# Performance work log

Hardware: AMD Instinct MI355X
Metric: run time of the kernel (lower is better)

## Reference

```python
import jax, jax.numpy as jnp
import numpy as np
from math import factorial

# (mul, l, parity) in mul_ir layout order
IRREPS_IN1 = [(128, 0, 1), (128, 1, -1), (128, 2, 1)]
IRREPS_IN2 = [(1, 0, 1), (1, 1, -1), (1, 2, 1)]
IRREPS_OUT = [(128, 0, 1), (128, 1, -1), (128, 2, 1)]
BATCH = 65536


def _f(n):
    return float(factorial(int(round(n))))


def _su2_cg(j1, j2, j3, m1, m2, m3):
    # <j1 m1 j2 m2 | j3 m3> (Racah formula, complex SU(2) basis)
    if m3 != m1 + m2:
        return 0.0
    vmin = int(max(-j1 + j2 + m3, -j1 + m1, 0))
    vmax = int(min(j2 + j3 + m1, j3 - j1 + j2, j3 + m3))
    C = ((2 * j3 + 1) * _f(j3 + j1 - j2) * _f(j3 - j1 + j2) * _f(j1 + j2 - j3)
         * _f(j3 + m3) * _f(j3 - m3)
         / (_f(j1 + j2 + j3 + 1) * _f(j1 - m1) * _f(j1 + m1) * _f(j2 - m2) * _f(j2 + m2))) ** 0.5
    S = 0.0
    for v in range(vmin, vmax + 1):
        S += (-1.0) ** (v + j2 + m2) * _f(j2 + j3 + m1 - v) * _f(j1 - m1 + v) / (
            _f(v) * _f(j3 - j1 + j2 - v) * _f(j3 + m3 - v) * _f(v + j1 - j2 - m3))
    return C * S


def _q(l):
    # change of basis real -> complex spherical harmonics (e3nn convention)
    q = np.zeros((2 * l + 1, 2 * l + 1), dtype=np.complex128)
    for m in range(-l, 0):
        q[l + m, l + abs(m)] = 1 / np.sqrt(2)
        q[l + m, l - abs(m)] = -1j / np.sqrt(2)
    q[l, l] = 1.0
    for m in range(1, l + 1):
        q[l + m, l + abs(m)] = (-1) ** m / np.sqrt(2)
        q[l + m, l - abs(m)] = 1j * (-1) ** m / np.sqrt(2)
    return (-1j) ** l * q


def _wigner_3j(l1, l2, l3):
    C = np.zeros((2 * l1 + 1, 2 * l2 + 1, 2 * l3 + 1))
    for m1 in range(-l1, l1 + 1):
        for m2 in range(-l2, l2 + 1):
            for m3 in range(-l3, l3 + 1):
                C[l1 + m1, l2 + m2, l3 + m3] = _su2_cg(l1, l2, l3, m1, m2, m3)
    Q1, Q2, Q3 = _q(l1), _q(l2), _q(l3)
    R = np.einsum('ij,kl,nm,ikn->jlm', Q1, Q2, np.conj(Q3), C.astype(np.complex128))
    return np.real(R) / np.sqrt(2 * l3 + 1)  # sum of squares == 1 (3j normalization)


def _slices(irreps):
    out, off = [], 0
    for mul, l, _ in irreps:
        out.append((off, mul, 2 * l + 1))
        off += mul * (2 * l + 1)
    return out, off


S1, DIM1 = _slices(IRREPS_IN1)
S2, DIM2 = _slices(IRREPS_IN2)
S3, DIM3 = _slices(IRREPS_OUT)

# fully-connected instruction list: all parity/triangle-allowed (i1, i2, i3) paths
_instr = [(i1, i2, i3)
          for i1, (_, l1, p1) in enumerate(IRREPS_IN1)
          for i2, (_, l2, p2) in enumerate(IRREPS_IN2)
          for i3, (_, l3, p3) in enumerate(IRREPS_OUT)
          if p1 * p2 == p3 and abs(l1 - l2) <= l3 <= l1 + l2]

# path normalization 'element': fan-in per output irrep = sum of mul1*mul2 over incoming paths
_fan = {}
for i1, i2, i3 in _instr:
    _fan[i3] = _fan.get(i3, 0) + IRREPS_IN1[i1][0] * IRREPS_IN2[i2][0]

PATHS, _off = [], 0
for i1, i2, i3 in _instr:
    mu1, l1, _ = IRREPS_IN1[i1]
    mu2, l2, _ = IRREPS_IN2[i2]
    mu3, l3, _ = IRREPS_OUT[i3]
    # irrep_normalization 'component' + path 'element': path_weight = sqrt((2l3+1)/fan)
    cg = _wigner_3j(l1, l2, l3) * np.sqrt((2 * l3 + 1) / _fan[i3])
    PATHS.append((i1, i2, i3, _off, (mu1, mu2, mu3), jnp.asarray(cg, dtype=jnp.float32)))
    _off += mu1 * mu2 * mu3
WEIGHT_NUMEL = _off  # 180224 for these irreps (11 paths x 128*1*128)


def _fctp(x1, x2, weight):
    w = weight.reshape(-1).astype(x1.dtype)
    acc = [None] * len(IRREPS_OUT)
    for i1, i2, i3, off, wshape, cg in PATHS:
        o1, mu1, d1 = S1[i1]
        o2, mu2, d2 = S2[i2]
        a = x1[:, o1:o1 + mu1 * d1].reshape(-1, mu1, d1)  # [B, u, i]
        b = x2[:, o2:o2 + mu2 * d2].reshape(-1, mu2, d2)  # [B, v, j]
        wp = w[off:off + wshape[0] * wshape[1] * wshape[2]].reshape(wshape)  # [u, v, w]
        c = jnp.einsum('bui,bvj,uvw,ijk->bwk', a, b, wp, cg.astype(x1.dtype))
        acc[i3] = c if acc[i3] is None else acc[i3] + c
    # mul_ir layout: flatten each (B, mul, 2l+1) segment and concatenate
    return jnp.concatenate([s.reshape(s.shape[0], -1) for s in acc], axis=-1)


def setup_inputs():
    key = jax.random.key(0)
    k1, k2, k3 = jax.random.split(key, 3)
    return {
        "x1": jax.random.normal(k1, (BATCH, DIM1), dtype=jnp.float32),
        "x2": jax.random.normal(k2, (BATCH, DIM2), dtype=jnp.float32),
        "weight": jax.random.normal(k3, (1, WEIGHT_NUMEL), dtype=jnp.float32),
    }


def reference(x1, x2, weight):
    return _fctp(x1, x2, weight)
```

## Files before the change

kernel.cpp:

```cpp
#include <hip/hip_runtime.h>
#include <hip/hip_bf16.h>

typedef __attribute__((ext_vector_type(8))) short bf16x8;
typedef __attribute__((ext_vector_type(4))) float f32x4;
typedef __attribute__((ext_vector_type(4))) unsigned int u32x4;
typedef __attribute__((ext_vector_type(2))) unsigned int u32x2;
typedef __attribute__((ext_vector_type(4))) unsigned short u16x4;

__device__ __forceinline__ unsigned short f2bf(float f) {
  __hip_bfloat16 h = __float2bfloat16(f);
  return __builtin_bit_cast(unsigned short, h);
}
__device__ __forceinline__ float bfw(unsigned int word, int hi) {
  union { unsigned int i; float f; } v;
  v.i = hi ? (word & 0xffff0000u) : (word << 16);
  return v.f;
}

struct cplx { double re, im; };
__device__ __forceinline__ cplx cmul(cplx a, cplx b) {
  return {a.re * b.re - a.im * b.im, a.re * b.im + a.im * b.re};
}
__device__ __forceinline__ double fct_(int n) {
  const double f[8] = {1., 1., 2., 6., 24., 120., 720., 5040.};
  return f[n];
}
__device__ __forceinline__ int imax_(int a, int b) { return a > b ? a : b; }
__device__ __forceinline__ int imin_(int a, int b) { return a < b ? a : b; }

__device__ double su2_cg(int j1, int j2, int j3, int m1, int m2, int m3) {
  if (m3 != m1 + m2) return 0.0;
  int vmin = imax_(imax_(-j1 + j2 + m3, -j1 + m1), 0);
  int vmax = imin_(imin_(j2 + j3 + m1, j3 - j1 + j2), j3 + m3);
  double C = sqrt((2.0 * j3 + 1.0) * fct_(j3 + j1 - j2) * fct_(j3 - j1 + j2) * fct_(j1 + j2 - j3)
                  * fct_(j3 + m3) * fct_(j3 - m3)
                  / (fct_(j1 + j2 + j3 + 1) * fct_(j1 - m1) * fct_(j1 + m1) * fct_(j2 - m2) * fct_(j2 + m2)));
  double S = 0.0;
  for (int v = vmin; v <= vmax; ++v) {
    double sgn = ((v + j2 + m2) & 1) ? -1.0 : 1.0;
    S += sgn * fct_(j2 + j3 + m1 - v) * fct_(j1 - m1 + v)
         / (fct_(v) * fct_(j3 - j1 + j2 - v) * fct_(j3 + m3 - v) * fct_(v + j1 - j2 - m3));
  }
  return C * S;
}

__device__ cplx q_entry(int l, int r, int c) {
  const double s2 = 0.70710678118654752440;
  int m = r - l;
  cplx v = {0.0, 0.0};
  if (m < 0) {
    if (c == l - m) v = {s2, 0.0};
    else if (c == l + m) v = {0.0, -s2};
  } else if (m == 0) {
    if (c == l) v = {1.0, 0.0};
  } else {
    double sgn = (m & 1) ? -1.0 : 1.0;
    if (c == l + m) v = {sgn * s2, 0.0};
    else if (c == l - m) v = {0.0, sgn * s2};
  }
  cplx f;
  switch (l & 3) {
    case 0: f = {1.0, 0.0}; break;
    case 1: f = {0.0, -1.0}; break;
    case 2: f = {-1.0, 0.0}; break;
    default: f = {0.0, 1.0}; break;
  }
  return cmul(f, v);
}

__global__ void init_kernel(const float* __restrict__ w, unsigned short* __restrict__ Wt,
                            float* __restrict__ cgw, float* __restrict__ gfold,
                            unsigned int* __restrict__ gmap) {
  const int blk = blockIdx.x;
  const int tid = threadIdx.x;
  if (blk < 704) {
    int g = blk * 256 + tid;
    int p = g >> 14, rem = g & 16383;
    int u = rem >> 7, wc = rem & 127;
    Wt[(p << 14) + (wc << 7) + u] = f2bf(w[g]);
    return;
  }
  if (blk == 715) {
    if (tid < 115) {
      const int PBt[12] = {0,1,4,9,18,21,36,45,70,85,90,115};
      const int O2t[11] = {0,1,4,0,1,1,4,0,1,4,4};
      int p = 0;
      while (tid >= PBt[p + 1]) ++p;
      gmap[tid] = O2t[p];
    }
    return;
  }
  __shared__ float s_cg[125];
  const int p = blk - 704;
  const int L1t[11] = {0,0,0,1,1,1,1,2,2,2,2};
  const int L2t[11] = {0,1,2,0,1,1,2,0,1,2,2};
  const int L3t[11] = {0,1,2,1,0,2,1,2,1,0,2};
  const int PBt[11] = {0,1,4,9,18,21,36,45,70,85,90};
  const double FAN[11] = {384.,512.,512.,512.,384.,512.,512.,512.,512.,384.,512.};
  const int l1 = L1t[p], l2 = L2t[p], l3 = L3t[p];
  const int n1 = 2 * l1 + 1, n2 = 2 * l2 + 1, n3 = 2 * l3 + 1;
  if (tid < n1 * n2 * n3) {
    const int a = tid / (n2 * n3), b = (tid / n3) % n2, c = tid % n3;
    double sre = 0.0;
    for (int i = 0; i < n1; ++i)
      for (int k = 0; k < n2; ++k)
        for (int n = 0; n < n3; ++n) {
          double cg = su2_cg(l1, l2, l3, i - l1, k - l2, n - l3);
          if (cg == 0.0) continue;
          cplx q1 = q_entry(l1, i, a);
          cplx q2 = q_entry(l2, k, b);
          cplx q3 = q_entry(l3, n, c);
          q3.im = -q3.im;
          cplx pr = cmul(cmul(q1, q2), q3);
          sre += pr.re * cg;
        }
    float val = (float)(sre / sqrt(FAN[p]));
    s_cg[a * 25 + b * 5 + c] = val;
    cgw[p * 125 + a * 25 + b * 5 + c] = val;
  }
  __syncthreads();
  if (tid < n1 * n3) {
    int i = tid / n3, k = tid % n3;
    for (int j = 0; j < 5; ++j)
      gfold[(PBt[p] + tid) * 5 + j] = (j < n2) ? s_cg[i * 25 + j * 5 + k] : 0.f;
  }
}

__device__ __forceinline__ void stage_all(const float* __restrict__ x1, int Mbase,
                                          unsigned short* __restrict__ s_a) {
  const int tid = threadIdx.x;
#pragma unroll 4
  for (int rep = 0; rep < 18; ++rep) {
    int it = tid + rep * 256;
    int row = it / 288, c4 = it % 288;
    int col = c4 << 2;
    const f32x4 v = __builtin_nontemporal_load(
        (const f32x4*)&x1[(size_t)(Mbase + row) * 1152 + col]);
    unsigned short* sr = s_a + row * 128;
    if (col < 128) {
      u16x4 h;
#pragma unroll
      for (int q = 0; q < 4; ++q) h[q] = f2bf(v[q]);
      *(u16x4*)&sr[(((col >> 3) ^ row) << 3) + (col & 7)] = h;
    } else if (col < 512) {
      int cc = col - 128;
#pragma unroll
      for (int q = 0; q < 4; ++q) {
        int u = (cc + q) / 3, i = (cc + q) % 3;
        s_a[(1 + i) * 2048 + row * 128 + (((u >> 3) ^ row) << 3) + (u & 7)] = f2bf(v[q]);
      }
    } else {
      int cc = col - 512;
#pragma unroll
      for (int q = 0; q < 4; ++q) {
        int u = (cc + q) / 5, i = (cc + q) % 5;
        s_a[(4 + i) * 2048 + row * 128 + (((u >> 3) ^ row) << 3) + (u & 7)] = f2bf(v[q]);
      }
    }
  }
}

template<int PID, int L1, int L3, int PBASE>
__device__ __forceinline__ void do_path(const unsigned short* __restrict__ s_a,
                                        const unsigned short* __restrict__ s_g,
                                        const unsigned short* __restrict__ Wt,
                                        int kg, int r16, int nbase,
                                        f32x4 (&acc)[2 * L3 + 1][2]) {
  constexpr int D1 = 2 * L1 + 1, D3 = 2 * L3 + 1;
  constexpr int GB = (L1 == 0) ? 0 : ((L1 == 1) ? 2048 : 8192);
  const unsigned short* __restrict__ wbase = Wt + (PID << 14);
  u32x4 bw[2][4];
#pragma unroll
  for (int nf = 0; nf < 2; ++nf)
#pragma unroll
    for (int us = 0; us < 4; ++us)
      bw[nf][us] = *(const u32x4*)&wbase[(nbase + nf * 16 + r16) * 128 + us * 32 + kg * 8];
  const unsigned short* __restrict__ ap0 = s_a + GB + r16 * 128;
  auto gread = [&](int e) -> f32x4 {
    const u32x2 gd = *(const u32x2*)&s_g[(e << 4) + (kg << 2)];
    f32x4 r;
    r[0] = bfw(gd.x, 0); r[1] = bfw(gd.x, 1);
    r[2] = bfw(gd.y, 0); r[3] = bfw(gd.y, 1);
    return r;
  };
#pragma unroll 1
  for (int ii = 0; ii + 1 < D1; ii += 2) {
    const unsigned short* apA = ap0 + ii * 2048;
    const unsigned short* apB = apA + 2048;
    f32x4 y0[2][2] = {{f32x4{0.f,0.f,0.f,0.f}, f32x4{0.f,0.f,0.f,0.f}},
                      {f32x4{0.f,0.f,0.f,0.f}, f32x4{0.f,0.f,0.f,0.f}}};
    f32x4 y1[2][2] = {{f32x4{0.f,0.f,0.f,0.f}, f32x4{0.f,0.f,0.f,0.f}},
                      {f32x4{0.f,0.f,0.f,0.f}, f32x4{0.f,0.f,0.f,0.f}}};
#pragma unroll
    for (int us = 0; us < 4; ++us) {
      const int soff = (((us * 4 + kg) ^ r16) << 3);
      const u32x4 a0 = *(const u32x4*)(apA + soff);
      const u32x4 a1 = *(const u32x4*)(apB + soff);
      const int h = us & 1;
#pragma unroll
      for (int nf = 0; nf < 2; ++nf) {
        y0[nf][h] = __builtin_amdgcn_mfma_f32_16x16x32_bf16(
            __builtin_bit_cast(bf16x8, a0), __builtin_bit_cast(bf16x8, bw[nf][us]),
            y0[nf][h], 0, 0, 0);
        y1[nf][h] = __builtin_amdgcn_mfma_f32_16x16x32_bf16(
            __builtin_bit_cast(bf16x8, a1), __builtin_bit_cast(bf16x8, bw[nf][us]),
            y1[nf][h], 0, 0, 0);
      }
    }
#pragma unroll
    for (int k = 0; k < D3; ++k) {
      const f32x4 gA = gread(PBASE + ii * D3 + k);
      const f32x4 gB = gread(PBASE + (ii + 1) * D3 + k);
#pragma unroll
      for (int nf = 0; nf < 2; ++nf) {
        acc[k][nf] += gA * (y0[nf][0] + y0[nf][1]);
        acc[k][nf] += gB * (y1[nf][0] + y1[nf][1]);
      }
    }
  }
  if (D1 & 1) {
    constexpr int it = D1 - 1;
    const unsigned short* ap = ap0 + it * 2048;
    f32x4 y[2][2] = {{f32x4{0.f,0.f,0.f,0.f}, f32x4{0.f,0.f,0.f,0.f}},
                     {f32x4{0.f,0.f,0.f,0.f}, f32x4{0.f,0.f,0.f,0.f}}};
#pragma unroll
    for (int us = 0; us < 4; ++us) {
      const int soff = (((us * 4 + kg) ^ r16) << 3);
      const u32x4 af = *(const u32x4*)(ap + soff);
      const int h = us & 1;
#pragma unroll
      for (int nf = 0; nf < 2; ++nf)
        y[nf][h] = __builtin_amdgcn_mfma_f32_16x16x32_bf16(
            __builtin_bit_cast(bf16x8, af), __builtin_bit_cast(bf16x8, bw[nf][us]),
            y[nf][h], 0, 0, 0);
    }
#pragma unroll
    for (int k = 0; k < D3; ++k) {
      const f32x4 g4 = gread(PBASE + it * D3 + k);
#pragma unroll
      for (int nf = 0; nf < 2; ++nf) acc[k][nf] += g4 * (y[nf][0] + y[nf][1]);
    }
  }
}

__global__ void __launch_bounds__(256, 2) fctp_main(
    const float* __restrict__ x1, const float* __restrict__ x2,
    const float* __restrict__ gfold, const unsigned int* __restrict__ gmap,
    const unsigned short* __restrict__ Wt, float* __restrict__ out) {
  __shared__ __align__(16) unsigned short s_a[18432];
  __shared__ __align__(16) unsigned short s_g[1840];
  const int tid = threadIdx.x;
  const int Mbase = blockIdx.x << 4;

  stage_all(x1, Mbase, s_a);

  {
    const int row = tid & 15, e0 = tid >> 4;
    const float* __restrict__ xr = x2 + (size_t)(Mbase + row) * 9;
    float x2r[9];
#pragma unroll
    for (int j = 0; j < 9; ++j) x2r[j] = xr[j];
#pragma unroll
    for (int it = 0; it < 8; ++it) {
      const int e = e0 + it * 16;
      if (e < 115) {
        const int o2 = (int)gmap[e];
        const float* __restrict__ gf = gfold + e * 5;
        float s = 0.f;
#pragma unroll
        for (int j = 0; j < 5; ++j) s += gf[j] * x2r[o2 + j];
        s_g[(e << 4) + row] = f2bf(s);
      }
    }
  }

  const int lane = tid & 63, ni = tid >> 6;
  const int r16 = lane & 15, kg = lane >> 4;
  const int nbase = ni << 5;

  __syncthreads();

  const int bout = Mbase + (kg << 2);

  {
    f32x4 acc[1][2] = {};
    do_path<0, 0, 0, 0>(s_a, s_g, Wt, kg, r16, nbase, acc);
    do_path<4, 1, 0, 18>(s_a, s_g, Wt, kg, r16, nbase, acc);
    do_path<9, 2, 0, 85>(s_a, s_g, Wt, kg, r16, nbase, acc);
#pragma unroll
    for (int nf = 0; nf < 2; ++nf) {
      const int w = nbase + nf * 16 + r16;
#pragma unroll
      for (int r = 0; r < 4; ++r)
        __builtin_nontemporal_store(acc[0][nf][r],
                                    &out[(size_t)(bout + r) * 1152 + w]);
    }
  }
  {
    f32x4 acc[3][2] = {};
    do_path<1, 0, 1, 1>(s_a, s_g, Wt, kg, r16, nbase, acc);
    do_path<3, 1, 1, 9>(s_a, s_g, Wt, kg, r16, nbase, acc);
    do_path<6, 1, 1, 36>(s_a, s_g, Wt, kg, r16, nbase, acc);
    do_path<8, 2, 1, 70>(s_a, s_g, Wt, kg, r16, nbase, acc);
#pragma unroll
    for (int nf = 0; nf < 2; ++nf) {
      const int w = nbase + nf * 16 + r16;
#pragma unroll
      for (int r = 0; r < 4; ++r) {
        float* o = out + (size_t)(bout + r) * 1152 + 128 + w * 3;
#pragma unroll
        for (int k = 0; k < 3; ++k) o[k] = acc[k][nf][r];
      }
    }
  }
  {
    f32x4 acc[5][2] = {};
    do_path<2, 0, 2, 4>(s_a, s_g, Wt, kg, r16, nbase, acc);
    do_path<5, 1, 2, 21>(s_a, s_g, Wt, kg, r16, nbase, acc);
    do_path<7, 2, 2, 45>(s_a, s_g, Wt, kg, r16, nbase, acc);
    do_path<10, 2, 2, 90>(s_a, s_g, Wt, kg, r16, nbase, acc);
#pragma unroll
    for (int nf = 0; nf < 2; ++nf) {
      const int w = nbase + nf * 16 + r16;
#pragma unroll
      for (int r = 0; r < 4; ++r) {
        float* o = out + (size_t)(bout + r) * 1152 + 512 + w * 5;
#pragma unroll
        for (int k = 0; k < 5; ++k) o[k] = acc[k][nf][r];
      }
    }
  }
}

extern "C" void kernel_launch(void* const* d_in, const int* in_sizes, int n_in,
                              void* d_out, int out_size, void* d_ws, size_t ws_size,
                              hipStream_t stream) {
  (void)in_sizes; (void)n_in; (void)out_size; (void)ws_size;
  const float* x1 = (const float*)d_in[0];
  const float* x2 = (const float*)d_in[1];
  const float* w  = (const float*)d_in[2];
  float* out = (float*)d_out;
  float* cgw = (float*)d_ws;
  unsigned int* gmap = (unsigned int*)((char*)d_ws + 5504);
  float* gfold = (float*)((char*)d_ws + 6144);
  unsigned short* Wt = (unsigned short*)((char*)d_ws + 16384);
  init_kernel<<<dim3(716), dim3(256), 0, stream>>>(w, Wt, cgw, gfold, gmap);
  fctp_main<<<dim3(4096), dim3(256), 0, stream>>>(x1, x2, gfold, gmap, Wt, out);
}
```

Before: 330.8 us.

## Split output channels across two blocks per row tile, halving per-wave N work

```diff
diff --git a/kernel.cpp b/kernel.cpp
--- a/kernel.cpp
+++ b/kernel.cpp
@@ -134,8 +134,7 @@
     int it = tid + rep * 256;
     int row = it / 288, c4 = it % 288;
     int col = c4 << 2;
-    const f32x4 v = __builtin_nontemporal_load(
-        (const f32x4*)&x1[(size_t)(Mbase + row) * 1152 + col]);
+    const f32x4 v = *(const f32x4*)&x1[(size_t)(Mbase + row) * 1152 + col];
     unsigned short* sr = s_a + row * 128;
     if (col < 128) {
       u16x4 h;
@@ -165,16 +164,14 @@
                                         const unsigned short* __restrict__ s_g,
                                         const unsigned short* __restrict__ Wt,
                                         int kg, int r16, int nbase,
-                                        f32x4 (&acc)[2 * L3 + 1][2]) {
+                                        f32x4 (&acc)[2 * L3 + 1]) {
   constexpr int D1 = 2 * L1 + 1, D3 = 2 * L3 + 1;
   constexpr int GB = (L1 == 0) ? 0 : ((L1 == 1) ? 2048 : 8192);
   const unsigned short* __restrict__ wbase = Wt + (PID << 14);
-  u32x4 bw[2][4];
-#pragma unroll
-  for (int nf = 0; nf < 2; ++nf)
-#pragma unroll
-    for (int us = 0; us < 4; ++us)
-      bw[nf][us] = *(const u32x4*)&wbase[(nbase + nf * 16 + r16) * 128 + us * 32 + kg * 8];
+  u32x4 bw[4];
+#pragma unroll
+  for (int us = 0; us < 4; ++us)
+    bw[us] = *(const u32x4*)&wbase[(nbase + r16) * 128 + us * 32 + kg * 8];
   const unsigned short* __restrict__ ap0 = s_a + GB + r16 * 128;
   auto gread = [&](int e) -> f32x4 {
     const u32x2 gd = *(const u32x2*)&s_g[(e << 4) + (kg << 2)];
@@ -187,58 +184,46 @@
   for (int ii = 0; ii + 1 < D1; ii += 2) {
     const unsigned short* apA = ap0 + ii * 2048;
     const unsigned short* apB = apA + 2048;
-    f32x4 y0[2][2] = {{f32x4{0.f,0.f,0.f,0.f}, f32x4{0.f,0.f,0.f,0.f}},
-                      {f32x4{0.f,0.f,0.f,0.f}, f32x4{0.f,0.f,0.f,0.f}}};
-    f32x4 y1[2][2] = {{f32x4{0.f,0.f,0.f,0.f}, f32x4{0.f,0.f,0.f,0.f}},
-                      {f32x4{0.f,0.f,0.f,0.f}, f32x4{0.f,0.f,0.f,0.f}}};
+    f32x4 y0[2] = {f32x4{0.f,0.f,0.f,0.f}, f32x4{0.f,0.f,0.f,0.f}};
+    f32x4 y1[2] = {f32x4{0.f,0.f,0.f,0.f}, f32x4{0.f,0.f,0.f,0.f}};
 #pragma unroll
     for (int us = 0; us < 4; ++us) {
       const int soff = (((us * 4 + kg) ^ r16) << 3);
       const u32x4 a0 = *(const u32x4*)(apA + soff);
       const u32x4 a1 = *(const u32x4*)(apB + soff);
-      const int h = us & 1;
-#pragma unroll
-      for (int nf = 0; nf < 2; ++nf) {
-        y0[nf][h] = __builtin_amdgcn_mfma_f32_16x16x32_bf16(
-            __builtin_bit_cast(bf16x8, a0), __builtin_bit_cast(bf16x8, bw[nf][us]),
-            y0[nf][h], 0, 0, 0);
-        y1[nf][h] = __builtin_amdgcn_mfma_f32_16x16x32_bf16(
-            __builtin_bit_cast(bf16x8, a1), __builtin_bit_cast(bf16x8, bw[nf][us]),
-            y1[nf][h], 0, 0, 0);
-      }
+      const int hh = us & 1;
+      y0[hh] = __builtin_amdgcn_mfma_f32_16x16x32_bf16(
+          __builtin_bit_cast(bf16x8, a0), __builtin_bit_cast(bf16x8, bw[us]),
+          y0[hh], 0, 0, 0);
+      y1[hh] = __builtin_amdgcn_mfma_f32_16x16x32_bf16(
+          __builtin_bit_cast(bf16x8, a1), __builtin_bit_cast(bf16x8, bw[us]),
+          y1[hh], 0, 0, 0);
     }
 #pragma unroll
     for (int k = 0; k < D3; ++k) {
       const f32x4 gA = gread(PBASE + ii * D3 + k);
       const f32x4 gB = gread(PBASE + (ii + 1) * D3 + k);
-#pragma unroll
-      for (int nf = 0; nf < 2; ++nf) {
-        acc[k][nf] += gA * (y0[nf][0] + y0[nf][1]);
-        acc[k][nf] += gB * (y1[nf][0] + y1[nf][1]);
-      }
+      acc[k] += gA * (y0[0] + y0[1]);
+      acc[k] += gB * (y1[0] + y1[1]);
     }
   }
   if (D1 & 1) {
     constexpr int it = D1 - 1;
     const unsigned short* ap = ap0 + it * 2048;
-    f32x4 y[2][2] = {{f32x4{0.f,0.f,0.f,0.f}, f32x4{0.f,0.f,0.f,0.f}},
-                     {f32x4{0.f,0.f,0.f,0.f}, f32x4{0.f,0.f,0.f,0.f}}};
+    f32x4 y[2] = {f32x4{0.f,0.f,0.f,0.f}, f32x4{0.f,0.f,0.f,0.f}};
 #pragma unroll
     for (int us = 0; us < 4; ++us) {
       const int soff = (((us * 4 + kg) ^ r16) << 3);
       const u32x4 af = *(const u32x4*)(ap + soff);
-      const int h = us & 1;
-#pragma unroll
-      for (int nf = 0; nf < 2; ++nf)
-        y[nf][h] = __builtin_amdgcn_mfma_f32_16x16x32_bf16(
-            __builtin_bit_cast(bf16x8, af), __builtin_bit_cast(bf16x8, bw[nf][us]),
-            y[nf][h], 0, 0, 0);
+      const int hh = us & 1;
+      y[hh] = __builtin_amdgcn_mfma_f32_16x16x32_bf16(
+          __builtin_bit_cast(bf16x8, af), __builtin_bit_cast(bf16x8, bw[us]),
+          y[hh], 0, 0, 0);
     }
 #pragma unroll
     for (int k = 0; k < D3; ++k) {
       const f32x4 g4 = gread(PBASE + it * D3 + k);
-#pragma unroll
-      for (int nf = 0; nf < 2; ++nf) acc[k][nf] += g4 * (y[nf][0] + y[nf][1]);
+      acc[k] += g4 * (y[0] + y[1]);
     }
   }
 }
@@ -250,7 +235,8 @@
   __shared__ __align__(16) unsigned short s_a[18432];
   __shared__ __align__(16) unsigned short s_g[1840];
   const int tid = threadIdx.x;
-  const int Mbase = blockIdx.x << 4;
+  const int Mbase = (blockIdx.x >> 1) << 4;
+  const int hw = blockIdx.x & 1;
 
   stage_all(x1, Mbase, s_a);
 
@@ -276,58 +262,46 @@
 
   const int lane = tid & 63, ni = tid >> 6;
   const int r16 = lane & 15, kg = lane >> 4;
-  const int nbase = ni << 5;
+  const int nbase = (hw << 6) + (ni << 4);
 
   __syncthreads();
 
   const int bout = Mbase + (kg << 2);
+  const int w = nbase + r16;
 
   {
-    f32x4 acc[1][2] = {};
+    f32x4 acc[1] = {};
     do_path<0, 0, 0, 0>(s_a, s_g, Wt, kg, r16, nbase, acc);
     do_path<4, 1, 0, 18>(s_a, s_g, Wt, kg, r16, nbase, acc);
     do_path<9, 2, 0, 85>(s_a, s_g, Wt, kg, r16, nbase, acc);
 #pragma unroll
-    for (int nf = 0; nf < 2; ++nf) {
-      const int w = nbase + nf * 16 + r16;
-#pragma unroll
-      for (int r = 0; r < 4; ++r)
-        __builtin_nontemporal_store(acc[0][nf][r],
-                                    &out[(size_t)(bout + r) * 1152 + w]);
-    }
+    for (int r = 0; r < 4; ++r)
+      __builtin_nontemporal_store(acc[0][r], &out[(size_t)(bout + r) * 1152 + w]);
   }
   {
-    f32x4 acc[3][2] = {};
+    f32x4 acc[3] = {};
     do_path<1, 0, 1, 1>(s_a, s_g, Wt, kg, r16, nbase, acc);
     do_path<3, 1, 1, 9>(s_a, s_g, Wt, kg, r16, nbase, acc);
     do_path<6, 1, 1, 36>(s_a, s_g, Wt, kg, r16, nbase, acc);
     do_path<8, 2, 1, 70>(s_a, s_g, Wt, kg, r16, nbase, acc);
 #pragma unroll
-    for (int nf = 0; nf < 2; ++nf) {
-      const int w = nbase + nf * 16 + r16;
-#pragma unroll
-      for (int r = 0; r < 4; ++r) {
-        float* o = out + (size_t)(bout + r) * 1152 + 128 + w * 3;
-#pragma unroll
-        for (int k = 0; k < 3; ++k) o[k] = acc[k][nf][r];
-      }
+    for (int r = 0; r < 4; ++r) {
+      float* o = out + (size_t)(bout + r) * 1152 + 128 + w * 3;
+#pragma unroll
+      for (int k = 0; k < 3; ++k) o[k] = acc[k][r];
     }
   }
   {
-    f32x4 acc[5][2] = {};
+    f32x4 acc[5] = {};
     do_path<2, 0, 2, 4>(s_a, s_g, Wt, kg, r16, nbase, acc);
     do_path<5, 1, 2, 21>(s_a, s_g, Wt, kg, r16, nbase, acc);
     do_path<7, 2, 2, 45>(s_a, s_g, Wt, kg, r16, nbase, acc);
     do_path<10, 2, 2, 90>(s_a, s_g, Wt, kg, r16, nbase, acc);
 #pragma unroll
-    for (int nf = 0; nf < 2; ++nf) {
-      const int w = nbase + nf * 16 + r16;
-#pragma unroll
-      for (int r = 0; r < 4; ++r) {
-        float* o = out + (size_t)(bout + r) * 1152 + 512 + w * 5;
-#pragma unroll
-        for (int k = 0; k < 5; ++k) o[k] = acc[k][nf][r];
-      }
+    for (int r = 0; r < 4; ++r) {
+      float* o = out + (size_t)(bout + r) * 1152 + 512 + w * 5;
+#pragma unroll
+      for (int k = 0; k < 5; ++k) o[k] = acc[k][r];
     }
   }
 }
@@ -345,5 +319,5 @@
   float* gfold = (float*)((char*)d_ws + 6144);
   unsigned short* Wt = (unsigned short*)((char*)d_ws + 16384);
   init_kernel<<<dim3(716), dim3(256), 0, stream>>>(w, Wt, cgw, gfold, gmap);
-  fctp_main<<<dim3(4096), dim3(256), 0, stream>>>(x1, x2, gfold, gmap, Wt, out);
-}
+  fctp_main<<<dim3(8192), dim3(256), 0, stream>>>(x1, x2, gfold, gmap, Wt, out);
+}
```

Result: slower. 480.8 us (+45.3%).
